# Kernel tuning notes

Hardware: AMD Instinct MI355X
Metric: run time of the kernel (lower is better)

## Reference

```python
import jax, jax.numpy as jnp
import numpy as np

B, V, C = 8192, 512, 16  # batch, num_variables, constraints per variable
N1 = V + 1  # augmented with bias column


def setup_inputs() -> dict:
    key = jax.random.key(0)
    k1, k2, k3 = jax.random.split(key, 3)
    preds = jax.random.normal(k1, (B, V), dtype=jnp.float32)
    # Acyclic structure: variable v's constraints only reference earlier
    # variables (columns < v) plus the bias column (column V).
    cols = jnp.arange(N1)[None, :]              # [1, N1]
    vids = jnp.arange(V)[:, None]               # [V, 1]
    mask = ((cols < vids) | (cols == V)).astype(jnp.float32)[:, None, :]  # [V,1,N1]
    scale = 0.1
    pos_mats = jax.random.normal(k2, (V, C, N1), dtype=jnp.float32) * scale * mask
    neg_mats = jax.random.normal(k3, (V, C, N1), dtype=jnp.float32) * scale * mask
    return {"preds": preds, "pos_mats": pos_mats, "neg_mats": neg_mats}


def reference(preds, pos_mats, neg_mats):
    # Augment preds with a ones column (bias), as in the original __call__.
    b = preds.shape[0]
    p0 = jnp.concatenate([preds, jnp.ones((b, 1), preds.dtype)], axis=1)  # [B, N1]
    var_ids = jnp.arange(pos_mats.shape[0])

    def step(p, xs):
        pm, nm, v = xs  # pm, nm: [C, N1]
        # apply_matrix: (preds * matrix).sum(-1) with max / min reduction over C
        lower = jnp.einsum('bn,cn->bc', p, pm).max(axis=1)  # [B]
        upper = jnp.einsum('bn,cn->bc', p, nm).min(axis=1)  # [B]
        # get_final_x_correction: clamp prediction into [lower, upper]
        corrected = jnp.minimum(jnp.maximum(p[:, v], lower), upper)
        p = p.at[:, v].set(corrected)
        return p, None

    pf, _ = jax.lax.scan(step, p0, (pos_mats, neg_mats, var_ids))
    return pf[:, : preds.shape[1]]
```

## Files before the change

kernel.cpp:

```cpp
#include <hip/hip_runtime.h>

#define BATCH 8192
#define V 512
#define N1 513
#define KCH 16
#define NCHUNKS 32
#define RB 32
#define NT 1024
#define PKS 520
#define SJP 772

typedef __bf16 bf16_t;
typedef bf16_t bf16x8 __attribute__((ext_vector_type(8)));
typedef float f32x4 __attribute__((ext_vector_type(4)));
typedef float f32x2 __attribute__((ext_vector_type(2)));

#define EPP 4194304ull
#define DV_OFF (EPP * 2ull)
#define BV_OFF (DV_OFF + 1048576ull)

__device__ __forceinline__ f32x4 mfma16(bf16x8 a, bf16x8 b, f32x4 c) {
    return __builtin_amdgcn_mfma_f32_16x16x32_bf16(a, b, c, 0, 0, 0);
}

__device__ __forceinline__ float bcast_lane(float x, int l) {
    return __int_as_float(__builtin_amdgcn_readlane(__float_as_int(x), l));
}

__device__ __forceinline__ float dpp_xor1_max(float x) {
    const int xi = __float_as_int(x);
    const float o = __int_as_float(
        __builtin_amdgcn_update_dpp(xi, xi, 0xB1, 0xF, 0xF, false));
    return fmaxf(x, o);
}

__global__ __launch_bounds__(1024)
void repack_all(const float* __restrict__ pos, const float* __restrict__ neg,
                bf16_t* __restrict__ Mhi, float* __restrict__ Dv,
                float* __restrict__ Bv)
{
    __shared__ float sb[2 * 256 * 36];
    const int bx  = blockIdx.x;
    const int tid = threadIdx.x;
    if (bx < 496) {
        const int cc  = (bx >> 4) + 1;
        const int kb  = bx & 15;
        const int nkb = (cc + 1) >> 1;
        if (kb >= nkb) return;
        const int klen = 16 * cc;
        for (int idx = tid; idx < 8192; idx += 1024) {
            const int r = idx >> 5, k32 = idx & 31;
            const int k = kb * 32 + k32;
            const size_t row = (size_t)cc * 256 + r;
            float xp = 0.0f, xn = 0.0f;
            if (k < klen) {
                xp = pos[row * N1 + k];
                xn = -neg[row * N1 + k];
            }
            sb[r * 36 + k32]            = xp;
            sb[256 * 36 + r * 36 + k32] = xn;
        }
        __syncthreads();
        const size_t base = 16384ull * (size_t)((cc * cc) / 4) + (size_t)kb * 16384ull;
        for (int e8 = tid; e8 < 2048; e8 += 1024) {
            const int t = e8 >> 6, s = e8 & 63;
            const int c = s & 15, q = s >> 4;
            const int vloc = t >> 1, m = t & 1;
            const float* sp = &sb[m * 256 * 36 + (vloc * 16 + c) * 36 + 8 * q];
            bf16x8 o;
            #pragma unroll
            for (int jj = 0; jj < 8; ++jj) o[jj] = (bf16_t)sp[jj];
            *(bf16x8*)(Mhi + base + (size_t)e8 * 8) = o;
        }
    } else {
        const int cc = bx - 496;
        float* bufP = sb;
        float* bufN = sb + 256 * 17;
        for (int idx = tid; idx < 4096; idx += 1024) {
            const int r = idx >> 4, kk = idx & 15;
            const size_t row = (size_t)(cc * 256 + r);
            bufP[r * 17 + kk] = pos[row * N1 + cc * 16 + kk];
            bufN[r * 17 + kk] = neg[row * N1 + cc * 16 + kk];
        }
        __syncthreads();
        for (int idx = tid; idx < 8192; idx += 1024) {
            const int vl = idx >> 9, j = idx & 511;
            const int vlo = j >> 5, c = j & 15;
            const int m = (j >> 4) & 1;
            const float x = (m ? bufN : bufP)[(vlo * 16 + c) * 17 + vl];
            Dv[(size_t)cc * 8192 + idx] = m ? -x : x;
        }
        for (int j = tid; j < 512; j += 1024) {
            const int vlo = j >> 5, c = j & 15;
            const int m = (j >> 4) & 1;
            const float* src = m ? neg : pos;
            const float x = src[(size_t)(cc * 256 + vlo * 16 + c) * N1 + V];
            Bv[(size_t)cc * 512 + j] = m ? -x : x;
        }
    }
}

__global__ __launch_bounds__(NT, 4)
void shield_fused(const float* __restrict__ preds,
                  const bf16_t* __restrict__ Mhi,
                  const float* __restrict__ Dv, const float* __restrict__ Bv,
                  float* __restrict__ out)
{
    __shared__ bf16_t Phi[RB * PKS];
    __shared__ float  S[RB * SJP];

    const int tid  = threadIdx.x;
    const int b0   = blockIdx.x * RB;
    const int lane = tid & 63;
    const int w    = tid >> 6;
    const int cq   = lane & 15;
    const int q    = lane >> 4;
    const int rp0  = w * 2;

    {
        const int r = tid >> 5, seg = tid & 31;
        const float* prow = preds + (size_t)(b0 + r) * V + seg * 16;
        #pragma unroll
        for (int k = 0; k < 16; k += 4) {
            const float4 p4 = *(const float4*)(prow + k);
            const int n = seg * 16 + k;
            Phi[r * PKS + n + 0] = (bf16_t)p4.x;
            Phi[r * PKS + n + 1] = (bf16_t)p4.y;
            Phi[r * PKS + n + 2] = (bf16_t)p4.z;
            Phi[r * PKS + n + 3] = (bf16_t)p4.w;
        }
    }

    int tJ[2], sct[2];
    #pragma unroll
    for (int tt = 0; tt < 2; ++tt) {
        tJ[tt]  = ((2 * w + tt) << 4) + cq;
        sct[tt] = 12 * (tJ[tt] >> 3) + (tJ[tt] & 7);
    }
    const int aoff0 = cq * PKS + 8 * q;
    const int aoff1 = (16 + cq) * PKS + 8 * q;

    f32x4 acc[2][2];
    #pragma unroll
    for (int tt = 0; tt < 2; ++tt) {
        const float b = Bv[tJ[tt]];
        acc[0][tt] = f32x4{b, b, b, b};
        acc[1][tt] = f32x4{b, b, b, b};
    }

    #pragma unroll 1
    for (int cc = 0; cc < NCHUNKS; ++cc) {
        const int v0 = cc * 16;
        const int  ccn  = cc + 1;
        const bool hasN = ccn < NCHUNKS;
        const int  nkbN = hasN ? ((ccn + 1) >> 1) : 0;
        const bf16_t* phN = Mhi + 16384ull * (size_t)((ccn * ccn) / 4)
                          + (size_t)lane * 8 + (size_t)(2 * w) * 512;

        #pragma unroll
        for (int tt = 0; tt < 2; ++tt)
            #pragma unroll
            for (int reg = 0; reg < 4; ++reg) {
                S[(4 * q + reg) * SJP + sct[tt]]      = acc[0][tt][reg];
                S[(16 + 4 * q + reg) * SJP + sct[tt]] = acc[1][tt][reg];
            }
        __syncthreads();

        f32x2 s2[8];
        {
            const float* sp = &S[rp0 * SJP + 12 * lane];
            const float4 a0 = *(const float4*)(sp);
            const float4 a1 = *(const float4*)(sp + 4);
            const float4 c0 = *(const float4*)(sp + SJP);
            const float4 c1 = *(const float4*)(sp + SJP + 4);
            s2[0] = f32x2{a0.x, c0.x}; s2[1] = f32x2{a0.y, c0.y};
            s2[2] = f32x2{a0.z, c0.z}; s2[3] = f32x2{a0.w, c0.w};
            s2[4] = f32x2{a1.x, c1.x}; s2[5] = f32x2{a1.y, c1.y};
            s2[6] = f32x2{a1.z, c1.z}; s2[7] = f32x2{a1.w, c1.w};
        }

        const bf16x8 poA0 = *(const bf16x8*)(Phi + rp0 * PKS + v0);
        const bf16x8 poA1 = *(const bf16x8*)(Phi + rp0 * PKS + v0 + 8);
        const bf16x8 poB0 = *(const bf16x8*)(Phi + (rp0 + 1) * PKS + v0);
        const bf16x8 poB1 = *(const bf16x8*)(Phi + (rp0 + 1) * PKS + v0 + 8);

        if (hasN) {
            #pragma unroll
            for (int tt = 0; tt < 2; ++tt) {
                const float b = Bv[(ccn << 9) + tJ[tt]];
                acc[0][tt] = f32x4{b, b, b, b};
                acc[1][tt] = f32x4{b, b, b, b};
            }
        }

        __syncthreads();

        {
            const float* src = Dv + (((size_t)cc * 16 + w) << 9) + 8 * lane;
            const float4 a = *(const float4*)(src);
            const float4 b = *(const float4*)(src + 4);
            float* dst = S + w * 512 + 8 * lane;
            *(float4*)(dst)     = a;
            *(float4*)(dst + 4) = b;
        }
        __syncthreads();

        #pragma unroll
        for (int vl = 0; vl < KCH; ++vl) {
            const int vcur = v0 + vl;
            const bool doKb = hasN && (vl < nkbN - 1);

            bf16x8 fa0, fa1, fb0, fb1;
            if (doKb) {
                const int k0 = vl * 32;
                fa0 = *(const bf16x8*)(Phi + aoff0 + k0);
                fa1 = *(const bf16x8*)(Phi + aoff1 + k0);
                const bf16_t* pb = phN + (size_t)k0 * 512;
                fb0 = *(const bf16x8*)(pb);
                fb1 = *(const bf16x8*)(pb + 512);
            }

            float dv[8];
            {
                const float* dls = S + vl * 512 + 8 * lane;
                const float4 d0 = *(const float4*)(dls);
                const float4 d1 = *(const float4*)(dls + 4);
                dv[0]=d0.x; dv[1]=d0.y; dv[2]=d0.z; dv[3]=d0.w;
                dv[4]=d1.x; dv[5]=d1.y; dv[6]=d1.z; dv[7]=d1.w;
            }
            const float po_[2] = {
                (float)(vl < 8 ? poA0[vl & 7] : poA1[vl & 7]),
                (float)(vl < 8 ? poB0[vl & 7] : poB1[vl & 7])
            };

            float red[2];
            #pragma unroll
            for (int r = 0; r < 2; ++r) {
                const float m0 = fmaxf(fmaxf(s2[0][r], s2[1][r]), s2[2][r]);
                const float m1 = fmaxf(fmaxf(s2[3][r], s2[4][r]), s2[5][r]);
                const float m2 = fmaxf(s2[6][r], s2[7][r]);
                const float mxr = fmaxf(fmaxf(m0, m1), m2);
                red[r] = dpp_xor1_max(mxr);
            }
            float pc[2];
            #pragma unroll
            for (int r = 0; r < 2; ++r) {
                const float lw  = bcast_lane(red[r], 4 * vl);
                const float nup = bcast_lane(red[r], 4 * vl + 2);
                pc[r] = fminf(fmaxf(po_[r], lw), -nup);
            }
            if (lane == 4 * vl) {
                Phi[rp0 * PKS + vcur]       = (bf16_t)pc[0];
                Phi[(rp0 + 1) * PKS + vcur] = (bf16_t)pc[1];
            }
            const f32x2 pcv = {pc[0], pc[1]};
            #pragma unroll
            for (int jj = 0; jj < 8; ++jj) {
                const f32x2 dsp = {dv[jj], dv[jj]};
                s2[jj] = __builtin_elementwise_fma(dsp, pcv, s2[jj]);
            }

            if (doKb) {
                acc[0][0] = mfma16(fa0, fb0, acc[0][0]);
                acc[1][0] = mfma16(fa1, fb0, acc[1][0]);
                acc[0][1] = mfma16(fa0, fb1, acc[0][1]);
                acc[1][1] = mfma16(fa1, fb1, acc[1][1]);
            }
        }

        __syncthreads();

        if (hasN) {
            const int k0 = (nkbN - 1) * 32;
            const bf16x8 fa0 = *(const bf16x8*)(Phi + aoff0 + k0);
            const bf16x8 fa1 = *(const bf16x8*)(Phi + aoff1 + k0);
            const bf16_t* pb = phN + (size_t)k0 * 512;
            const bf16x8 fb0 = *(const bf16x8*)(pb);
            const bf16x8 fb1 = *(const bf16x8*)(pb + 512);
            acc[0][0] = mfma16(fa0, fb0, acc[0][0]);
            acc[1][0] = mfma16(fa1, fb0, acc[1][0]);
            acc[0][1] = mfma16(fa0, fb1, acc[0][1]);
            acc[1][1] = mfma16(fa1, fb1, acc[1][1]);
        }
    }

    {
        const int r = tid >> 5, seg = tid & 31;
        float* orow = out + (size_t)(b0 + r) * V + seg * 16;
        #pragma unroll
        for (int k = 0; k < 16; k += 4) {
            const int n = seg * 16 + k;
            float4 o;
            o.x = (float)Phi[r * PKS + n + 0];
            o.y = (float)Phi[r * PKS + n + 1];
            o.z = (float)Phi[r * PKS + n + 2];
            o.w = (float)Phi[r * PKS + n + 3];
            *(float4*)(orow + k) = o;
        }
    }
}

extern "C" void kernel_launch(void* const* d_in, const int* in_sizes, int n_in,
                              void* d_out, int out_size, void* d_ws, size_t ws_size,
                              hipStream_t stream) {
    const float* preds = (const float*)d_in[0];
    const float* pos   = (const float*)d_in[1];
    const float* neg   = (const float*)d_in[2];
    float* o = (float*)d_out;
    char* base = (char*)d_ws;
    bf16_t* Mhi = (bf16_t*)base;
    float*  Dv  = (float*)(base + DV_OFF);
    float*  Bv  = (float*)(base + BV_OFF);
    repack_all<<<dim3(528), 1024, 0, stream>>>(pos, neg, Mhi, Dv, Bv);
    shield_fused<<<dim3(BATCH / RB), NT, 0, stream>>>(preds, Mhi, Dv, Bv, o);
}
```

Measured before the change: 379.1 us.

## Prefetch MFMA B-fragments into LDS via async global_load_lds double buffering

Replaces the direct global loads of the next-chunk matrix fragments with asynchronous global-to-LDS copies into per-wave double buffers. Each copy is issued one step ahead and gated by vmcnt waits, so global latency can overlap the serial clamp loop. The S scratch layout is also compacted (a smaller padded stride without the interleaved column mapping) to make room in LDS. This adds LDS pressure and relies on hand-written waitcnt ordering, and the new stride may cause bank conflicts.

```diff
diff --git a/kernel.cpp b/kernel.cpp
--- a/kernel.cpp
+++ b/kernel.cpp
@@ -8,7 +8,7 @@
 #define RB 32
 #define NT 1024
 #define PKS 520
-#define SJP 772
+#define SJ2 516
 
 typedef __bf16 bf16_t;
 typedef bf16_t bf16x8 __attribute__((ext_vector_type(8)));
@@ -32,6 +32,12 @@
     const float o = __int_as_float(
         __builtin_amdgcn_update_dpp(xi, xi, 0xB1, 0xF, 0xF, false));
     return fmaxf(x, o);
+}
+
+__device__ __forceinline__ void gload_lds16(const bf16_t* g, bf16_t* l) {
+    __builtin_amdgcn_global_load_lds(
+        (const __attribute__((address_space(1))) void*)g,
+        (__attribute__((address_space(3))) void*)l, 16, 0, 0);
 }
 
 __global__ __launch_bounds__(1024)
@@ -107,7 +113,8 @@
                   float* __restrict__ out)
 {
     __shared__ bf16_t Phi[RB * PKS];
-    __shared__ float  S[RB * SJP];
+    __shared__ float  S[RB * SJ2];
+    __shared__ bf16_t fbB[16384];
 
     const int tid  = threadIdx.x;
     const int b0   = blockIdx.x * RB;
@@ -116,6 +123,10 @@
     const int cq   = lane & 15;
     const int q    = lane >> 4;
     const int rp0  = w * 2;
+
+    bf16_t* const fbA = (bf16_t*)(S + 8192);
+    bf16_t* const myB = fbB + w * 1024;
+    bf16_t* const myA = fbA + w * 1024;
 
     {
         const int r = tid >> 5, seg = tid & 31;
@@ -131,12 +142,9 @@
         }
     }
 
-    int tJ[2], sct[2];
+    int tJ[2];
     #pragma unroll
-    for (int tt = 0; tt < 2; ++tt) {
-        tJ[tt]  = ((2 * w + tt) << 4) + cq;
-        sct[tt] = 12 * (tJ[tt] >> 3) + (tJ[tt] & 7);
-    }
+    for (int tt = 0; tt < 2; ++tt) tJ[tt] = ((2 * w + tt) << 4) + cq;
     const int aoff0 = cq * PKS + 8 * q;
     const int aoff1 = (16 + cq) * PKS + 8 * q;
 
@@ -161,18 +169,18 @@
         for (int tt = 0; tt < 2; ++tt)
             #pragma unroll
             for (int reg = 0; reg < 4; ++reg) {
-                S[(4 * q + reg) * SJP + sct[tt]]      = acc[0][tt][reg];
-                S[(16 + 4 * q + reg) * SJP + sct[tt]] = acc[1][tt][reg];
+                S[(4 * q + reg) * SJ2 + tJ[tt]]      = acc[0][tt][reg];
+                S[(16 + 4 * q + reg) * SJ2 + tJ[tt]] = acc[1][tt][reg];
             }
         __syncthreads();
 
         f32x2 s2[8];
         {
-            const float* sp = &S[rp0 * SJP + 12 * lane];
+            const float* sp = &S[rp0 * SJ2 + 8 * lane];
             const float4 a0 = *(const float4*)(sp);
             const float4 a1 = *(const float4*)(sp + 4);
-            const float4 c0 = *(const float4*)(sp + SJP);
-            const float4 c1 = *(const float4*)(sp + SJP + 4);
+            const float4 c0 = *(const float4*)(sp + SJ2);
+            const float4 c1 = *(const float4*)(sp + SJ2 + 4);
             s2[0] = f32x2{a0.x, c0.x}; s2[1] = f32x2{a0.y, c0.y};
             s2[2] = f32x2{a0.z, c0.z}; s2[3] = f32x2{a0.w, c0.w};
             s2[4] = f32x2{a1.x, c1.x}; s2[5] = f32x2{a1.y, c1.y};
@@ -203,6 +211,11 @@
             *(float4*)(dst)     = a;
             *(float4*)(dst + 4) = b;
         }
+        if (hasN) {
+            bf16_t* lb = ((nkbN - 1) & 1) ? myA : myB;
+            gload_lds16(phN,       lb);
+            gload_lds16(phN + 512, lb + 512);
+        }
         __syncthreads();
 
         #pragma unroll
@@ -212,12 +225,19 @@
 
             bf16x8 fa0, fa1, fb0, fb1;
             if (doKb) {
+                {
+                    bf16_t* lb = ((nkbN - vl) & 1) ? myA : myB;
+                    const bf16_t* g = phN + (size_t)(vl + 1) * 16384;
+                    gload_lds16(g,       lb);
+                    gload_lds16(g + 512, lb + 512);
+                }
+                asm volatile("s_waitcnt vmcnt(2)" ::: "memory");
+                const bf16_t* lb = ((nkbN - 1 - vl) & 1) ? myA : myB;
+                fb0 = *(const bf16x8*)(lb + lane * 8);
+                fb1 = *(const bf16x8*)(lb + 512 + lane * 8);
                 const int k0 = vl * 32;
                 fa0 = *(const bf16x8*)(Phi + aoff0 + k0);
                 fa1 = *(const bf16x8*)(Phi + aoff1 + k0);
-                const bf16_t* pb = phN + (size_t)k0 * 512;
-                fb0 = *(const bf16x8*)(pb);
-                fb1 = *(const bf16x8*)(pb + 512);
             }
 
             float dv[8];
@@ -271,12 +291,13 @@
         __syncthreads();
 
         if (hasN) {
+            asm volatile("s_waitcnt vmcnt(0)" ::: "memory");
             const int k0 = (nkbN - 1) * 32;
+            const bf16_t* lb = myB;
+            const bf16x8 fb0 = *(const bf16x8*)(lb + lane * 8);
+            const bf16x8 fb1 = *(const bf16x8*)(lb + 512 + lane * 8);
             const bf16x8 fa0 = *(const bf16x8*)(Phi + aoff0 + k0);
             const bf16x8 fa1 = *(const bf16x8*)(Phi + aoff1 + k0);
-            const bf16_t* pb = phN + (size_t)k0 * 512;
-            const bf16x8 fb0 = *(const bf16x8*)(pb);
-            const bf16x8 fb1 = *(const bf16x8*)(pb + 512);
             acc[0][0] = mfma16(fa0, fb0, acc[0][0]);
             acc[1][0] = mfma16(fa1, fb0, acc[1][0]);
             acc[0][1] = mfma16(fa0, fb1, acc[0][1]);
```

Result: slower. 397.4 us (+4.8%).
